# Kernel tuning notes

Measured on AMD Instinct MI355X. Metric: run time of the kernel, lower is better.

Reference implementation:

```python
import jax, jax.numpy as jnp
import numpy as np

# Dims
B, S, D = 2, 2048, 1024
H, KV = 16, 4            # rosa heads / kv heads -> n_rep = 4
QKB, VB = 16, 32          # query-key bits / value bits
N_REP = H // KV
TAU = 1.0


def setup_inputs() -> dict:
    key = jax.random.key(0)
    ks = jax.random.split(key, 8)
    sc = lambda fan_in: 1.0 / np.sqrt(fan_in)
    return {
        "hidden_states": jax.random.normal(ks[0], (B, S, D), jnp.float32),
        # Linear weights stored (in, out) so y = x @ W
        "Wq": jax.random.normal(ks[1], (D, H * QKB), jnp.float32) * sc(D),
        "Wk": jax.random.normal(ks[2], (D, KV * QKB), jnp.float32) * sc(D),
        "Wv": jax.random.normal(ks[3], (D, KV * VB), jnp.float32) * sc(D),
        "Wo": jax.random.normal(ks[4], (H * VB, D), jnp.float32) * sc(H * VB),
        "v_emb0": jnp.full((H * VB,), -1e-05, jnp.float32),
        "v_emb1": jnp.full((H * VB,), +1e-05, jnp.float32),
    }


def _repeat_kv(x, n_rep):
    # x: [B, KV, S, d] -> [B, KV*n_rep, S, d]
    b, kv, s, d = x.shape
    return jnp.broadcast_to(x[:, :, None], (b, kv, n_rep, s, d)).reshape(b, kv * n_rep, s, d)


def reference(hidden_states, Wq, Wk, Wv, Wo, v_emb0, v_emb1):
    b, s, _ = hidden_states.shape
    q = (hidden_states @ Wq).reshape(b, s, H, QKB).transpose(0, 2, 1, 3)   # [B,H,S,QKB]
    k = (hidden_states @ Wk).reshape(b, s, KV, QKB).transpose(0, 2, 1, 3)
    v = (hidden_states @ Wv).reshape(b, s, KV, VB).transpose(0, 2, 1, 3)
    k = _repeat_kv(k, N_REP)                                               # [B,H,S,QKB]
    v = _repeat_kv(v, N_REP)                                               # [B,H,S,VB]

    # Soft binarization (hard path uses (x > 0); soft path relaxes with sigmoid(x/tau)).
    pq = jax.nn.sigmoid(q / TAU)
    pk = jax.nn.sigmoid(k / TAU)
    pv = jax.nn.sigmoid(v / TAU)

    # Expected number of matching bits between soft-binary q_i and k_j:
    # sum_b [ pq*pk + (1-pq)(1-pk) ] = QKB - sum(pq) - sum(pk) + 2 * pq.pk
    dot = jnp.einsum("bhsd,bhtd->bhst", pq, pk)                            # [B,H,S,S]
    scores = QKB - pq.sum(-1)[:, :, :, None] - pk.sum(-1)[:, :, None, :] + 2.0 * dot

    causal = jnp.tril(jnp.ones((s, s), bool))                              # [S,S]
    scores = jnp.where(causal[None, None], scores, jnp.finfo(scores.dtype).min)
    attn = jax.nn.softmax(scores / TAU, axis=-1)

    vh = jnp.einsum("bhst,bhtd->bhsd", attn, pv)                           # [B,H,S,VB]
    e0 = v_emb0.reshape(1, H, 1, VB)
    e1 = v_emb1.reshape(1, H, 1, VB)
    out = e0 * (1.0 - vh) + e1 * vh                                        # [B,H,S,VB]
    out = out.transpose(0, 2, 1, 3).reshape(b, s, H * VB)
    return out @ Wo                                                        # [B,S,D]
```

## Files before the change

### kernel.cpp

```cpp
#include <hip/hip_runtime.h>
#include <hip/hip_bf16.h>

#define B_    2
#define S_    2048
#define D_    1024
#define H_    16
#define KV_   4
#define QKB_  16
#define VB_   32
#define NTOK  (B_ * S_)
#define L2E_  1.44269504088896f

typedef __attribute__((ext_vector_type(8))) short bshort8;
typedef __attribute__((ext_vector_type(4))) float f32x4;

__device__ __forceinline__ unsigned short bf16_rne(float x) {
    unsigned u = __float_as_uint(x);
    return (unsigned short)((u + 0x7FFFu + ((u >> 16) & 1u)) >> 16);
}
__device__ __forceinline__ unsigned bf16x2_rne(float lo, float hi) {
    return (unsigned)bf16_rne(lo) | ((unsigned)bf16_rne(hi) << 16);
}
__device__ __forceinline__ float sum2bf(unsigned u) {
    return __uint_as_float(u << 16) + __uint_as_float(u & 0xFFFF0000u);
}
__device__ __forceinline__ void stage16(const unsigned short* g, unsigned short* l) {
    __builtin_amdgcn_global_load_lds(
        (const __attribute__((address_space(1))) void*)g,
        (__attribute__((address_space(3))) void*)l, 16, 0, 0);
}

__global__ __launch_bounds__(256) void cvt_hs_kernel(
    const float* __restrict__ src, unsigned short* __restrict__ dst)
{
    int i = blockIdx.x * 256 + threadIdx.x;
    const float4* s = (const float4*)src;
    float4 a = s[2 * i], b = s[2 * i + 1];
    uint4 o;
    o.x = bf16x2_rne(a.x, a.y); o.y = bf16x2_rne(a.z, a.w);
    o.z = bf16x2_rne(b.x, b.y); o.w = bf16x2_rne(b.z, b.w);
    ((uint4*)dst)[i] = o;
}

__global__ __launch_bounds__(256) void trans_w_kernel(
    const float* __restrict__ Wq, const float* __restrict__ Wk,
    const float* __restrict__ Wv, const float* __restrict__ Wo,
    unsigned short* __restrict__ Wcat_t, unsigned short* __restrict__ Wot)
{
    __shared__ float T[64][65];
    const int bid = blockIdx.x, t = threadIdx.x;
    const float* src; unsigned short* dst; int K, N, tk, tn, drow0;
    if (bid < 64)       { src = Wq; dst = Wcat_t; K = 1024; N = 256;  int r = bid;       tk = r & 15; tn = r >> 4; drow0 = 0; }
    else if (bid < 80)  { src = Wk; dst = Wcat_t; K = 1024; N = 64;   int r = bid - 64;  tk = r;      tn = 0;      drow0 = 256; }
    else if (bid < 112) { src = Wv; dst = Wcat_t; K = 1024; N = 128;  int r = bid - 80;  tk = r & 15; tn = r >> 4; drow0 = 320; }
    else                { src = Wo; dst = Wot;    K = 512;  N = 1024; int r = bid - 112; tk = r & 7;  tn = r >> 3; drow0 = 0; }
    const int k0 = tk * 64, n0 = tn * 64;
    const int rr = t >> 4, cc = (t & 15) * 4;
    #pragma unroll
    for (int i = 0; i < 4; ++i) {
        float4 v = *(const float4*)(src + (k0 + rr + i * 16) * N + n0 + cc);
        T[rr + i * 16][cc + 0] = v.x; T[rr + i * 16][cc + 1] = v.y;
        T[rr + i * 16][cc + 2] = v.z; T[rr + i * 16][cc + 3] = v.w;
    }
    __syncthreads();
    const int nloc = t >> 2, kc = (t & 3) * 16;
    unsigned o[8];
    #pragma unroll
    for (int j = 0; j < 8; ++j)
        o[j] = bf16x2_rne(T[kc + 2 * j][nloc], T[kc + 2 * j + 1][nloc]);
    unsigned short* dp = dst + (drow0 + n0 + nloc) * K + k0 + kc;
    uint4 w0; w0.x = o[0]; w0.y = o[1]; w0.z = o[2]; w0.w = o[3];
    uint4 w1; w1.x = o[4]; w1.y = o[5]; w1.z = o[6]; w1.w = o[7];
    *(uint4*)(dp) = w0;
    *(uint4*)(dp + 8) = w1;
}

__global__ __launch_bounds__(256, 2) void proj_gemm(
    const unsigned short* __restrict__ Ab, const unsigned short* __restrict__ Btb,
    unsigned short* __restrict__ qg, unsigned short* __restrict__ pko,
    unsigned short* __restrict__ pvT)
{
    __shared__ unsigned short As[64 * 64];
    __shared__ unsigned short Bs[128 * 64];
    const int tid = threadIdx.x, l = tid & 63, w = tid >> 6;
    const int l15 = l & 15, quad = l >> 4;
    const int m0 = blockIdx.x * 64, n0 = blockIdx.y * 128;
    const int wr = w & 1, wc = w >> 1;
    const int sr8 = l >> 3, sc8 = l & 7;
    f32x4 c[2][4];
    #pragma unroll
    for (int i = 0; i < 2; ++i)
        #pragma unroll
        for (int j = 0; j < 4; ++j) c[i][j] = (f32x4){0.f, 0.f, 0.f, 0.f};

    for (int k0 = 0; k0 < 1024; k0 += 64) {
        {
            int R0 = w * 8, r0 = R0 + sr8;
            stage16(Ab + (m0 + r0) * 1024 + k0 + (sc8 ^ (r0 & 7)) * 8, &As[R0 * 64]);
            int R1 = 32 + w * 8, r1 = R1 + sr8;
            stage16(Ab + (m0 + r1) * 1024 + k0 + (sc8 ^ (r1 & 7)) * 8, &As[R1 * 64]);
        }
        #pragma unroll
        for (int j = 0; j < 4; ++j) {
            int R = j * 32 + w * 8, r = R + sr8;
            stage16(Btb + (n0 + r) * 1024 + k0 + (sc8 ^ (r & 7)) * 8, &Bs[R * 64]);
        }
        __syncthreads();
        #pragma unroll
        for (int kh = 0; kh < 2; ++kh) {
            bshort8 a[2], b[4];
            #pragma unroll
            for (int ar = 0; ar < 2; ++ar) {
                int row = wr * 32 + ar * 16 + l15;
                a[ar] = *(const bshort8*)&As[row * 64 + (((kh * 4 + quad) ^ (row & 7)) * 8)];
            }
            #pragma unroll
            for (int bc = 0; bc < 4; ++bc) {
                int row = wc * 64 + bc * 16 + l15;
                b[bc] = *(const bshort8*)&Bs[row * 64 + (((kh * 4 + quad) ^ (row & 7)) * 8)];
            }
            #pragma unroll
            for (int ar = 0; ar < 2; ++ar)
                #pragma unroll
                for (int bc = 0; bc < 4; ++bc)
                    c[ar][bc] = __builtin_amdgcn_mfma_f32_16x16x32_bf16(a[ar], b[bc], c[ar][bc], 0, 0, 0);
        }
        __syncthreads();
    }

    #pragma unroll
    for (int ar = 0; ar < 2; ++ar)
        #pragma unroll
        for (int bc = 0; bc < 4; ++bc) {
            f32x4 v = c[ar][bc];
            const int n = n0 + wc * 64 + bc * 16 + l15;
            if (n >= 448) continue;
            const int tok0 = m0 + wr * 32 + ar * 16 + quad * 4;
            float sg[4];
            #pragma unroll
            for (int r = 0; r < 4; ++r)
                sg[r] = 1.f / (1.f + exp2f(-v[r] * L2E_));
            if (n < 256) {
                const int hh = n >> 4, d = n & 15;
                #pragma unroll
                for (int r = 0; r < 4; ++r) {
                    int tok = tok0 + r, bb = tok >> 11, ss = tok & 2047;
                    qg[(((bb * 16 + hh) * 2048) + ss) * 16 + d] =
                        bf16_rne(L2E_ * (2.f * sg[r] - 1.f));
                }
            } else if (n < 320) {
                const int j = n - 256, kvv = j >> 4, d = j & 15;
                #pragma unroll
                for (int r = 0; r < 4; ++r) {
                    int tok = tok0 + r, bb = tok >> 11, ss = tok & 2047;
                    pko[(((bb * 4 + kvv) * 2048) + ss) * 16 + d] = bf16_rne(sg[r]);
                }
            } else {
                const int j = n - 320, kvv = j >> 5, d = j & 31;
                const int bb = tok0 >> 11, ss = tok0 & 2047;
                const int tl = ss >> 6, ccol = ss & 63;
                uint2 wv; wv.x = bf16x2_rne(sg[0], sg[1]); wv.y = bf16x2_rne(sg[2], sg[3]);
                *(uint2*)(pvT + ((((bb * 4 + kvv) * 32) + tl) * 32 + d) * 64 + ccol) = wv;
            }
        }
}

__global__ __launch_bounds__(256, 2) void outproj_gemm(
    const unsigned short* __restrict__ Ab, const unsigned short* __restrict__ Btb,
    float* __restrict__ out)
{
    __shared__ unsigned short As[128 * 64];
    __shared__ unsigned short Bs[128 * 64];
    const int tid = threadIdx.x, l = tid & 63, w = tid >> 6;
    const int l15 = l & 15, quad = l >> 4;
    const int m0 = blockIdx.x * 128, n0 = blockIdx.y * 128;
    const int wr = w & 1, wc = w >> 1;
    const int sr8 = l >> 3, sc8 = l & 7;
    f32x4 c[4][4];
    #pragma unroll
    for (int i = 0; i < 4; ++i)
        #pragma unroll
        for (int j = 0; j < 4; ++j) c[i][j] = (f32x4){0.f, 0.f, 0.f, 0.f};

    for (int k0 = 0; k0 < 512; k0 += 64) {
        #pragma unroll
        for (int j = 0; j < 4; ++j) {
            int R = j * 32 + w * 8, r = R + sr8;
            stage16(Ab  + (m0 + r) * 512 + k0 + (sc8 ^ (r & 7)) * 8, &As[R * 64]);
            stage16(Btb + (n0 + r) * 512 + k0 + (sc8 ^ (r & 7)) * 8, &Bs[R * 64]);
        }
        __syncthreads();
        #pragma unroll
        for (int kh = 0; kh < 2; ++kh) {
            bshort8 a[4], b[4];
            #pragma unroll
            for (int ar = 0; ar < 4; ++ar) {
                int row = wr * 64 + ar * 16 + l15;
                a[ar] = *(const bshort8*)&As[row * 64 + (((kh * 4 + quad) ^ (row & 7)) * 8)];
            }
            #pragma unroll
            for (int bc = 0; bc < 4; ++bc) {
                int row = wc * 64 + bc * 16 + l15;
                b[bc] = *(const bshort8*)&Bs[row * 64 + (((kh * 4 + quad) ^ (row & 7)) * 8)];
            }
            #pragma unroll
            for (int ar = 0; ar < 4; ++ar)
                #pragma unroll
                for (int bc = 0; bc < 4; ++bc)
                    c[ar][bc] = __builtin_amdgcn_mfma_f32_16x16x32_bf16(a[ar], b[bc], c[ar][bc], 0, 0, 0);
        }
        __syncthreads();
    }

    #pragma unroll
    for (int ar = 0; ar < 4; ++ar)
        #pragma unroll
        for (int bc = 0; bc < 4; ++bc) {
            f32x4 v = c[ar][bc];
            const int col = n0 + wc * 64 + bc * 16 + l15;
            const int r0 = m0 + wr * 64 + ar * 16 + quad * 4;
            #pragma unroll
            for (int r = 0; r < 4; ++r)
                out[(r0 + r) * D_ + col] = v[r];
        }
}

struct AttnLDS {
    unsigned short Kt[2][64][24];
    unsigned short qg[64][24];
    unsigned short P[4][16][88];
};

__global__ __launch_bounds__(256, 4) void attn_kernel(
    const unsigned short* __restrict__ qg_g, const unsigned short* __restrict__ pk_g,
    const unsigned short* __restrict__ pvT_g, const float* __restrict__ e0,
    const float* __restrict__ e1, unsigned short* __restrict__ xo)
{
    __shared__ AttnLDS L;
    const int tid = threadIdx.x, l = tid & 63, wq = tid >> 6;
    const int l15 = l & 15, quad = l >> 4;
    const int g = blockIdx.x;
    const int idx = g & 255, kg = g >> 8;
    const int bh = idx & 31, rr = idx >> 5;
    int qt;
    if      (kg == 0) qt = rr;
    else if (kg == 1) qt = 31 - rr;
    else if (kg == 2) qt = 8 + rr;
    else              qt = 23 - rr;
    const int b = bh >> 4, h = bh & 15, kv = h >> 2;
    const int qbase = qt * 64;
    const unsigned short* pkb = pk_g + ((b * 4 + kv) * 2048) * 16;
    const unsigned short* pvb = pvT_g + (b * 4 + kv) * 65536;
    const unsigned short* qgb = qg_g + ((b * 16 + h) * 2048) * 16;

    const f32x4 zero4 = {0.f, 0.f, 0.f, 0.f};
    const bshort8 zero8 = {0, 0, 0, 0, 0, 0, 0, 0};

    if (tid < 128) {
        int row = tid >> 1, half = tid & 1;
        *(uint4*)&L.qg[row][half * 8] = *(const uint4*)(qgb + (qbase + row) * 16 + half * 8);
        uint4 cst; cst.x = 0x3F80u; cst.y = 0u; cst.z = 0u; cst.w = 0u;
        *(uint4*)&L.Kt[tid >> 6][tid & 63][16] = cst;
    } else {
        int t2 = tid - 128, row = t2 >> 1, half = t2 & 1;
        *(uint4*)&L.Kt[0][row][half * 8] = *(const uint4*)(pkb + row * 16 + half * 8);
    }
    if (tid < 64) {
        const uint4* qp = (const uint4*)(qgb + (qbase + tid) * 16);
        uint4 u0 = qp[0], u1 = qp[1];
        float s = sum2bf(u0.x) + sum2bf(u0.y) + sum2bf(u0.z) + sum2bf(u0.w)
                + sum2bf(u1.x) + sum2bf(u1.y) + sum2bf(u1.z) + sum2bf(u1.w);
        uint4 sv; sv.x = (unsigned)bf16_rne(-8.f * L2E_ - 0.5f * s);
        sv.y = 0u; sv.z = 0u; sv.w = 0u;
        *(uint4*)&L.qg[tid][16] = sv;
    }
    __syncthreads();

    bshort8 qfrag = zero8;
    if (quad < 3) qfrag = *(const bshort8*)&L.qg[wq * 16 + l15][quad * 8];

    f32x4 acc0 = zero4, acc1 = zero4;
    float lsum = 0.f;

    for (int t = 0; t < qt; ++t) {
        if (tid < 128) {
            int row = tid >> 1, half = tid & 1;
            *(uint4*)&L.Kt[(t + 1) & 1][row][half * 8] =
                *(const uint4*)(pkb + ((t + 1) * 64 + row) * 16 + half * 8);
        }
        const unsigned short* Kb = &L.Kt[t & 1][0][0];
        const unsigned short* vb = pvb + t * 2048 + l15 * 64 + quad * 8;
        bshort8 vlo0 = *(const bshort8*)(vb);
        bshort8 vlo1 = *(const bshort8*)(vb + 32);
        bshort8 vhi0 = *(const bshort8*)(vb + 1024);
        bshort8 vhi1 = *(const bshort8*)(vb + 1056);

        f32x4 sc[4];
        #pragma unroll
        for (int ks = 0; ks < 4; ++ks) {
            bshort8 kf = zero8;
            if (quad < 3) kf = *(const bshort8*)(Kb + (ks * 16 + l15) * 24 + quad * 8);
            sc[ks] = __builtin_amdgcn_mfma_f32_16x16x32_bf16(kf, qfrag, zero4, 0, 0, 0);
        }
        #pragma unroll
        for (int ks = 0; ks < 4; ++ks) {
            float p0 = exp2f(sc[ks][0]), p1 = exp2f(sc[ks][1]);
            float p2 = exp2f(sc[ks][2]), p3 = exp2f(sc[ks][3]);
            lsum += p0 + p1 + p2 + p3;
            uint2 wv; wv.x = bf16x2_rne(p0, p1); wv.y = bf16x2_rne(p2, p3);
            *(uint2*)&L.P[wq][l15][ks * 16 + quad * 4] = wv;
        }
        {
            bshort8 pf0 = *(const bshort8*)&L.P[wq][l15][quad * 8];
            bshort8 pf1 = *(const bshort8*)&L.P[wq][l15][32 + quad * 8];
            acc0 = __builtin_amdgcn_mfma_f32_16x16x32_bf16(vlo0, pf0, acc0, 0, 0, 0);
            acc1 = __builtin_amdgcn_mfma_f32_16x16x32_bf16(vhi0, pf0, acc1, 0, 0, 0);
            acc0 = __builtin_amdgcn_mfma_f32_16x16x32_bf16(vlo1, pf1, acc0, 0, 0, 0);
            acc1 = __builtin_amdgcn_mfma_f32_16x16x32_bf16(vhi1, pf1, acc1, 0, 0, 0);
        }
        __syncthreads();
    }

    {
        const unsigned short* Kb = &L.Kt[qt & 1][0][0];
        const unsigned short* vb = pvb + qt * 2048 + l15 * 64 + quad * 8;
        bshort8 vlo0 = *(const bshort8*)(vb);
        bshort8 vlo1 = *(const bshort8*)(vb + 32);
        bshort8 vhi0 = *(const bshort8*)(vb + 1024);
        bshort8 vhi1 = *(const bshort8*)(vb + 1056);
        const int q_lane = qbase + wq * 16 + l15;

        f32x4 sc[4];
        #pragma unroll
        for (int ks = 0; ks < 4; ++ks) {
            bshort8 kf = zero8;
            if (quad < 3) kf = *(const bshort8*)(Kb + (ks * 16 + l15) * 24 + quad * 8);
            sc[ks] = __builtin_amdgcn_mfma_f32_16x16x32_bf16(kf, qfrag, zero4, 0, 0, 0);
        }
        #pragma unroll
        for (int ks = 0; ks < 4; ++ks) {
            float pv0[4];
            #pragma unroll
            for (int r = 0; r < 4; ++r) {
                const int tg = qbase + ks * 16 + quad * 4 + r;
                float pp = (tg <= q_lane) ? exp2f(sc[ks][r]) : 0.f;
                lsum += pp; pv0[r] = pp;
            }
            uint2 wv; wv.x = bf16x2_rne(pv0[0], pv0[1]); wv.y = bf16x2_rne(pv0[2], pv0[3]);
            *(uint2*)&L.P[wq][l15][ks * 16 + quad * 4] = wv;
        }
        {
            bshort8 pf0 = *(const bshort8*)&L.P[wq][l15][quad * 8];
            bshort8 pf1 = *(const bshort8*)&L.P[wq][l15][32 + quad * 8];
            acc0 = __builtin_amdgcn_mfma_f32_16x16x32_bf16(vlo0, pf0, acc0, 0, 0, 0);
            acc1 = __builtin_amdgcn_mfma_f32_16x16x32_bf16(vhi0, pf0, acc1, 0, 0, 0);
            acc0 = __builtin_amdgcn_mfma_f32_16x16x32_bf16(vlo1, pf1, acc0, 0, 0, 0);
            acc1 = __builtin_amdgcn_mfma_f32_16x16x32_bf16(vhi1, pf1, acc1, 0, 0, 0);
        }
    }

    lsum += __shfl_xor(lsum, 16);
    lsum += __shfl_xor(lsum, 32);
    const float inv = 1.f / lsum;

    float e0v[8], dEv[8];
    #pragma unroll
    for (int vs = 0; vs < 2; ++vs)
        #pragma unroll
        for (int r = 0; r < 4; ++r) {
            int idx2 = h * 32 + vs * 16 + quad * 4 + r;
            float a = e0[idx2];
            e0v[vs * 4 + r] = a; dEv[vs * 4 + r] = e1[idx2] - a;
        }
    const int tok = b * 2048 + qbase + wq * 16 + l15;
    float o0[4], o1[4];
    #pragma unroll
    for (int r = 0; r < 4; ++r) {
        o0[r] = e0v[r]     + dEv[r]     * (acc0[r] * inv);
        o1[r] = e0v[4 + r] + dEv[4 + r] * (acc1[r] * inv);
    }
    uint2 w0; w0.x = bf16x2_rne(o0[0], o0[1]); w0.y = bf16x2_rne(o0[2], o0[3]);
    uint2 w1; w1.x = bf16x2_rne(o1[0], o1[1]); w1.y = bf16x2_rne(o1[2], o1[3]);
    *(uint2*)(xo + tok * 512 + h * 32 + quad * 4)      = w0;
    *(uint2*)(xo + tok * 512 + h * 32 + 16 + quad * 4) = w1;
}

extern "C" void kernel_launch(void* const* d_in, const int* in_sizes, int n_in,
                              void* d_out, int out_size, void* d_ws, size_t ws_size,
                              hipStream_t stream)
{
    const float* hs = (const float*)d_in[0];
    const float* Wq = (const float*)d_in[1];
    const float* Wk = (const float*)d_in[2];
    const float* Wv = (const float*)d_in[3];
    const float* Wo = (const float*)d_in[4];
    const float* e0 = (const float*)d_in[5];
    const float* e1 = (const float*)d_in[6];
    float* out = (float*)d_out;

    char* ws = (char*)d_ws;
    unsigned short* hs_b   = (unsigned short*)(ws);
    unsigned short* xo     = (unsigned short*)(ws);
    unsigned short* Wcat_t = (unsigned short*)(ws + 8388608);
    unsigned short* Wot    = (unsigned short*)(ws + 8388608 + 917504);
    unsigned short* qg     = (unsigned short*)(ws + 10354688);
    unsigned short* pk     = (unsigned short*)(ws + 12451840);
    unsigned short* pvT    = (unsigned short*)(ws + 12976128);

    cvt_hs_kernel<<<2048, 256, 0, stream>>>(hs, hs_b);
    trans_w_kernel<<<240, 256, 0, stream>>>(Wq, Wk, Wv, Wo, Wcat_t, Wot);
    proj_gemm<<<dim3(64, 4), 256, 0, stream>>>(hs_b, Wcat_t, qg, pk, pvT);
    attn_kernel<<<1024, 256, 0, stream>>>(qg, pk, pvT, e0, e1, xo);
    outproj_gemm<<<dim3(32, 8), 256, 0, stream>>>(xo, Wot, out);
}
```

Measured before the change: 147.0 us.

## Merge prep kernels, retile projection GEMMs, and drop LDS staging in attention

Fuses the hidden-state conversion and weight-transpose kernels into a single prep launch to save one kernel launch. Retiles the QKV projection to 64x64 tiles on a 64x7 grid so no padded columns are computed, and halves the out-projection M tile to 64 on a 64x8 grid to launch more blocks. In the attention kernel, Q and K fragments are now read straight from global memory into registers instead of being staged through LDS, which removes the per-tile __syncthreads. The trade-offs are lower per-block data reuse in the GEMMs and reliance on cache for the K loads.

```diff
diff --git a/kernel.cpp b/kernel.cpp
--- a/kernel.cpp
+++ b/kernel.cpp
@@ -30,25 +30,26 @@
         (__attribute__((address_space(3))) void*)l, 16, 0, 0);
 }
 
-__global__ __launch_bounds__(256) void cvt_hs_kernel(
-    const float* __restrict__ src, unsigned short* __restrict__ dst)
-{
-    int i = blockIdx.x * 256 + threadIdx.x;
-    const float4* s = (const float4*)src;
-    float4 a = s[2 * i], b = s[2 * i + 1];
-    uint4 o;
-    o.x = bf16x2_rne(a.x, a.y); o.y = bf16x2_rne(a.z, a.w);
-    o.z = bf16x2_rne(b.x, b.y); o.w = bf16x2_rne(b.z, b.w);
-    ((uint4*)dst)[i] = o;
-}
-
-__global__ __launch_bounds__(256) void trans_w_kernel(
+__global__ __launch_bounds__(256) void prep_kernel(
+    const float* __restrict__ hs,
     const float* __restrict__ Wq, const float* __restrict__ Wk,
     const float* __restrict__ Wv, const float* __restrict__ Wo,
+    unsigned short* __restrict__ hs_b,
     unsigned short* __restrict__ Wcat_t, unsigned short* __restrict__ Wot)
 {
     __shared__ float T[64][65];
-    const int bid = blockIdx.x, t = threadIdx.x;
+    const int t = threadIdx.x;
+    if (blockIdx.x < 2048) {
+        int i = blockIdx.x * 256 + t;
+        const float4* s = (const float4*)hs;
+        float4 a = s[2 * i], b = s[2 * i + 1];
+        uint4 o;
+        o.x = bf16x2_rne(a.x, a.y); o.y = bf16x2_rne(a.z, a.w);
+        o.z = bf16x2_rne(b.x, b.y); o.w = bf16x2_rne(b.z, b.w);
+        ((uint4*)hs_b)[i] = o;
+        return;
+    }
+    const int bid = blockIdx.x - 2048;
     const float* src; unsigned short* dst; int K, N, tk, tn, drow0;
     if (bid < 64)       { src = Wq; dst = Wcat_t; K = 1024; N = 256;  int r = bid;       tk = r & 15; tn = r >> 4; drow0 = 0; }
     else if (bid < 80)  { src = Wk; dst = Wcat_t; K = 1024; N = 64;   int r = bid - 64;  tk = r;      tn = 0;      drow0 = 256; }
@@ -75,10 +76,80 @@
     *(uint4*)(dp + 8) = w1;
 }
 
-__global__ __launch_bounds__(256, 2) void proj_gemm(
+__global__ __launch_bounds__(256, 4) void proj_gemm(
     const unsigned short* __restrict__ Ab, const unsigned short* __restrict__ Btb,
     unsigned short* __restrict__ qg, unsigned short* __restrict__ pko,
     unsigned short* __restrict__ pvT)
+{
+    __shared__ unsigned short As[64 * 64];
+    __shared__ unsigned short Bs[64 * 64];
+    const int tid = threadIdx.x, l = tid & 63, w = tid >> 6;
+    const int l15 = l & 15, quad = l >> 4;
+    const int m0 = blockIdx.x * 64, n0 = blockIdx.y * 64;
+    const int sr8 = l >> 3, sc8 = l & 7;
+    f32x4 c[4];
+    #pragma unroll
+    for (int j = 0; j < 4; ++j) c[j] = (f32x4){0.f, 0.f, 0.f, 0.f};
+
+    for (int k0 = 0; k0 < 1024; k0 += 64) {
+        int R0 = w * 8, r0 = R0 + sr8;
+        int R1 = 32 + w * 8, r1 = R1 + sr8;
+        stage16(Ab  + (m0 + r0) * 1024 + k0 + (sc8 ^ (r0 & 7)) * 8, &As[R0 * 64]);
+        stage16(Ab  + (m0 + r1) * 1024 + k0 + (sc8 ^ (r1 & 7)) * 8, &As[R1 * 64]);
+        stage16(Btb + (n0 + r0) * 1024 + k0 + (sc8 ^ (r0 & 7)) * 8, &Bs[R0 * 64]);
+        stage16(Btb + (n0 + r1) * 1024 + k0 + (sc8 ^ (r1 & 7)) * 8, &Bs[R1 * 64]);
+        __syncthreads();
+        #pragma unroll
+        for (int kh = 0; kh < 2; ++kh) {
+            const int arow = w * 16 + l15;
+            bshort8 a = *(const bshort8*)&As[arow * 64 + (((kh * 4 + quad) ^ (arow & 7)) * 8)];
+            #pragma unroll
+            for (int bc = 0; bc < 4; ++bc) {
+                const int brow = bc * 16 + l15;
+                bshort8 b = *(const bshort8*)&Bs[brow * 64 + (((kh * 4 + quad) ^ (brow & 7)) * 8)];
+                c[bc] = __builtin_amdgcn_mfma_f32_16x16x32_bf16(a, b, c[bc], 0, 0, 0);
+            }
+        }
+        __syncthreads();
+    }
+
+    const int tok0 = m0 + w * 16 + quad * 4;
+    #pragma unroll
+    for (int bc = 0; bc < 4; ++bc) {
+        f32x4 v = c[bc];
+        const int n = n0 + bc * 16 + l15;
+        float sg[4];
+        #pragma unroll
+        for (int r = 0; r < 4; ++r)
+            sg[r] = 1.f / (1.f + exp2f(-v[r] * L2E_));
+        if (n < 256) {
+            const int hh = n >> 4, d = n & 15;
+            #pragma unroll
+            for (int r = 0; r < 4; ++r) {
+                int tok = tok0 + r, bb = tok >> 11, ss = tok & 2047;
+                qg[(((bb * 16 + hh) * 2048) + ss) * 16 + d] =
+                    bf16_rne(L2E_ * (2.f * sg[r] - 1.f));
+            }
+        } else if (n < 320) {
+            const int j = n - 256, kvv = j >> 4, d = j & 15;
+            #pragma unroll
+            for (int r = 0; r < 4; ++r) {
+                int tok = tok0 + r, bb = tok >> 11, ss = tok & 2047;
+                pko[(((bb * 4 + kvv) * 2048) + ss) * 16 + d] = bf16_rne(sg[r]);
+            }
+        } else {
+            const int j = n - 320, kvv = j >> 5, d = j & 31;
+            const int bb = tok0 >> 11, ss = tok0 & 2047;
+            const int tl = ss >> 6, ccol = ss & 63;
+            uint2 wv; wv.x = bf16x2_rne(sg[0], sg[1]); wv.y = bf16x2_rne(sg[2], sg[3]);
+            *(uint2*)(pvT + ((((bb * 4 + kvv) * 32) + tl) * 32 + d) * 64 + ccol) = wv;
+        }
+    }
+}
+
+__global__ __launch_bounds__(256, 2) void outproj_gemm(
+    const unsigned short* __restrict__ Ab, const unsigned short* __restrict__ Btb,
+    float* __restrict__ out)
 {
     __shared__ unsigned short As[64 * 64];
     __shared__ unsigned short Bs[128 * 64];
@@ -93,17 +164,16 @@
         #pragma unroll
         for (int j = 0; j < 4; ++j) c[i][j] = (f32x4){0.f, 0.f, 0.f, 0.f};
 
-    for (int k0 = 0; k0 < 1024; k0 += 64) {
-        {
-            int R0 = w * 8, r0 = R0 + sr8;
-            stage16(Ab + (m0 + r0) * 1024 + k0 + (sc8 ^ (r0 & 7)) * 8, &As[R0 * 64]);
-            int R1 = 32 + w * 8, r1 = R1 + sr8;
-            stage16(Ab + (m0 + r1) * 1024 + k0 + (sc8 ^ (r1 & 7)) * 8, &As[R1 * 64]);
+    for (int k0 = 0; k0 < 512; k0 += 64) {
+        #pragma unroll
+        for (int j = 0; j < 2; ++j) {
+            int R = w * 16 + j * 8, r = R + sr8;
+            stage16(Ab + (m0 + r) * 512 + k0 + (sc8 ^ (r & 7)) * 8, &As[R * 64]);
         }
         #pragma unroll
         for (int j = 0; j < 4; ++j) {
             int R = j * 32 + w * 8, r = R + sr8;
-            stage16(Btb + (n0 + r) * 1024 + k0 + (sc8 ^ (r & 7)) * 8, &Bs[R * 64]);
+            stage16(Btb + (n0 + r) * 512 + k0 + (sc8 ^ (r & 7)) * 8, &Bs[R * 64]);
         }
         __syncthreads();
         #pragma unroll
@@ -133,92 +203,8 @@
         #pragma unroll
         for (int bc = 0; bc < 4; ++bc) {
             f32x4 v = c[ar][bc];
-            const int n = n0 + wc * 64 + bc * 16 + l15;
-            if (n >= 448) continue;
-            const int tok0 = m0 + wr * 32 + ar * 16 + quad * 4;
-            float sg[4];
-            #pragma unroll
-            for (int r = 0; r < 4; ++r)
-                sg[r] = 1.f / (1.f + exp2f(-v[r] * L2E_));
-            if (n < 256) {
-                const int hh = n >> 4, d = n & 15;
-                #pragma unroll
-                for (int r = 0; r < 4; ++r) {
-                    int tok = tok0 + r, bb = tok >> 11, ss = tok & 2047;
-                    qg[(((bb * 16 + hh) * 2048) + ss) * 16 + d] =
-                        bf16_rne(L2E_ * (2.f * sg[r] - 1.f));
-                }
-            } else if (n < 320) {
-                const int j = n - 256, kvv = j >> 4, d = j & 15;
-                #pragma unroll
-                for (int r = 0; r < 4; ++r) {
-                    int tok = tok0 + r, bb = tok >> 11, ss = tok & 2047;
-                    pko[(((bb * 4 + kvv) * 2048) + ss) * 16 + d] = bf16_rne(sg[r]);
-                }
-            } else {
-                const int j = n - 320, kvv = j >> 5, d = j & 31;
-                const int bb = tok0 >> 11, ss = tok0 & 2047;
-                const int tl = ss >> 6, ccol = ss & 63;
-                uint2 wv; wv.x = bf16x2_rne(sg[0], sg[1]); wv.y = bf16x2_rne(sg[2], sg[3]);
-                *(uint2*)(pvT + ((((bb * 4 + kvv) * 32) + tl) * 32 + d) * 64 + ccol) = wv;
-            }
-        }
-}
-
-__global__ __launch_bounds__(256, 2) void outproj_gemm(
-    const unsigned short* __restrict__ Ab, const unsigned short* __restrict__ Btb,
-    float* __restrict__ out)
-{
-    __shared__ unsigned short As[128 * 64];
-    __shared__ unsigned short Bs[128 * 64];
-    const int tid = threadIdx.x, l = tid & 63, w = tid >> 6;
-    const int l15 = l & 15, quad = l >> 4;
-    const int m0 = blockIdx.x * 128, n0 = blockIdx.y * 128;
-    const int wr = w & 1, wc = w >> 1;
-    const int sr8 = l >> 3, sc8 = l & 7;
-    f32x4 c[4][4];
-    #pragma unroll
-    for (int i = 0; i < 4; ++i)
-        #pragma unroll
-        for (int j = 0; j < 4; ++j) c[i][j] = (f32x4){0.f, 0.f, 0.f, 0.f};
-
-    for (int k0 = 0; k0 < 512; k0 += 64) {
-        #pragma unroll
-        for (int j = 0; j < 4; ++j) {
-            int R = j * 32 + w * 8, r = R + sr8;
-            stage16(Ab  + (m0 + r) * 512 + k0 + (sc8 ^ (r & 7)) * 8, &As[R * 64]);
-            stage16(Btb + (n0 + r) * 512 + k0 + (sc8 ^ (r & 7)) * 8, &Bs[R * 64]);
-        }
-        __syncthreads();
-        #pragma unroll
-        for (int kh = 0; kh < 2; ++kh) {
-            bshort8 a[4], b[4];
-            #pragma unroll
-            for (int ar = 0; ar < 4; ++ar) {
-                int row = wr * 64 + ar * 16 + l15;
-                a[ar] = *(const bshort8*)&As[row * 64 + (((kh * 4 + quad) ^ (row & 7)) * 8)];
-            }
-            #pragma unroll
-            for (int bc = 0; bc < 4; ++bc) {
-                int row = wc * 64 + bc * 16 + l15;
-                b[bc] = *(const bshort8*)&Bs[row * 64 + (((kh * 4 + quad) ^ (row & 7)) * 8)];
-            }
-            #pragma unroll
-            for (int ar = 0; ar < 4; ++ar)
-                #pragma unroll
-                for (int bc = 0; bc < 4; ++bc)
-                    c[ar][bc] = __builtin_amdgcn_mfma_f32_16x16x32_bf16(a[ar], b[bc], c[ar][bc], 0, 0, 0);
-        }
-        __syncthreads();
-    }
-
-    #pragma unroll
-    for (int ar = 0; ar < 4; ++ar)
-        #pragma unroll
-        for (int bc = 0; bc < 4; ++bc) {
-            f32x4 v = c[ar][bc];
             const int col = n0 + wc * 64 + bc * 16 + l15;
-            const int r0 = m0 + wr * 64 + ar * 16 + quad * 4;
+            const int r0 = m0 + wr * 32 + ar * 16 + quad * 4;
             #pragma unroll
             for (int r = 0; r < 4; ++r)
                 out[(r0 + r) * D_ + col] = v[r];
@@ -226,8 +212,6 @@
 }
 
 struct AttnLDS {
-    unsigned short Kt[2][64][24];
-    unsigned short qg[64][24];
     unsigned short P[4][16][88];
 };
 
@@ -256,52 +240,38 @@
     const f32x4 zero4 = {0.f, 0.f, 0.f, 0.f};
     const bshort8 zero8 = {0, 0, 0, 0, 0, 0, 0, 0};
 
-    if (tid < 128) {
-        int row = tid >> 1, half = tid & 1;
-        *(uint4*)&L.qg[row][half * 8] = *(const uint4*)(qgb + (qbase + row) * 16 + half * 8);
-        uint4 cst; cst.x = 0x3F80u; cst.y = 0u; cst.z = 0u; cst.w = 0u;
-        *(uint4*)&L.Kt[tid >> 6][tid & 63][16] = cst;
-    } else {
-        int t2 = tid - 128, row = t2 >> 1, half = t2 & 1;
-        *(uint4*)&L.Kt[0][row][half * 8] = *(const uint4*)(pkb + row * 16 + half * 8);
-    }
-    if (tid < 64) {
-        const uint4* qp = (const uint4*)(qgb + (qbase + tid) * 16);
-        uint4 u0 = qp[0], u1 = qp[1];
-        float s = sum2bf(u0.x) + sum2bf(u0.y) + sum2bf(u0.z) + sum2bf(u0.w)
-                + sum2bf(u1.x) + sum2bf(u1.y) + sum2bf(u1.z) + sum2bf(u1.w);
-        uint4 sv; sv.x = (unsigned)bf16_rne(-8.f * L2E_ - 0.5f * s);
-        sv.y = 0u; sv.z = 0u; sv.w = 0u;
-        *(uint4*)&L.qg[tid][16] = sv;
-    }
-    __syncthreads();
-
+    const unsigned short* qrow = qgb + (qbase + wq * 16 + l15) * 16;
+    uint4 qu0 = *(const uint4*)qrow;
+    uint4 qu1 = *(const uint4*)(qrow + 8);
+    float s = sum2bf(qu0.x) + sum2bf(qu0.y) + sum2bf(qu0.z) + sum2bf(qu0.w)
+            + sum2bf(qu1.x) + sum2bf(qu1.y) + sum2bf(qu1.z) + sum2bf(qu1.w);
     bshort8 qfrag = zero8;
-    if (quad < 3) qfrag = *(const bshort8*)&L.qg[wq * 16 + l15][quad * 8];
+    if (quad == 0)      qfrag = __builtin_bit_cast(bshort8, qu0);
+    else if (quad == 1) qfrag = __builtin_bit_cast(bshort8, qu1);
+    else if (quad == 2) qfrag[0] = (short)bf16_rne(-8.f * L2E_ - 0.5f * s);
+
+    bshort8 kone = zero8; kone[0] = (short)0x3F80;
 
     f32x4 acc0 = zero4, acc1 = zero4;
     float lsum = 0.f;
 
     for (int t = 0; t < qt; ++t) {
-        if (tid < 128) {
-            int row = tid >> 1, half = tid & 1;
-            *(uint4*)&L.Kt[(t + 1) & 1][row][half * 8] =
-                *(const uint4*)(pkb + ((t + 1) * 64 + row) * 16 + half * 8);
-        }
-        const unsigned short* Kb = &L.Kt[t & 1][0][0];
+        const int t0 = t * 64;
+        f32x4 sc[4];
+        #pragma unroll
+        for (int ks = 0; ks < 4; ++ks) {
+            bshort8 kf;
+            if (quad < 2)       kf = *(const bshort8*)(pkb + (t0 + ks * 16 + l15) * 16 + quad * 8);
+            else if (quad == 2) kf = kone;
+            else                kf = zero8;
+            sc[ks] = __builtin_amdgcn_mfma_f32_16x16x32_bf16(kf, qfrag, zero4, 0, 0, 0);
+        }
         const unsigned short* vb = pvb + t * 2048 + l15 * 64 + quad * 8;
         bshort8 vlo0 = *(const bshort8*)(vb);
         bshort8 vlo1 = *(const bshort8*)(vb + 32);
         bshort8 vhi0 = *(const bshort8*)(vb + 1024);
         bshort8 vhi1 = *(const bshort8*)(vb + 1056);
 
-        f32x4 sc[4];
-        #pragma unroll
-        for (int ks = 0; ks < 4; ++ks) {
-            bshort8 kf = zero8;
-            if (quad < 3) kf = *(const bshort8*)(Kb + (ks * 16 + l15) * 24 + quad * 8);
-            sc[ks] = __builtin_amdgcn_mfma_f32_16x16x32_bf16(kf, qfrag, zero4, 0, 0, 0);
-        }
         #pragma unroll
         for (int ks = 0; ks < 4; ++ks) {
             float p0 = exp2f(sc[ks][0]), p1 = exp2f(sc[ks][1]);
@@ -318,31 +288,32 @@
             acc0 = __builtin_amdgcn_mfma_f32_16x16x32_bf16(vlo1, pf1, acc0, 0, 0, 0);
             acc1 = __builtin_amdgcn_mfma_f32_16x16x32_bf16(vhi1, pf1, acc1, 0, 0, 0);
         }
-        __syncthreads();
     }
 
     {
-        const unsigned short* Kb = &L.Kt[qt & 1][0][0];
+        const int t0 = qt * 64;
+        const int q_lane = qbase + wq * 16 + l15;
+        f32x4 sc[4];
+        #pragma unroll
+        for (int ks = 0; ks < 4; ++ks) {
+            bshort8 kf;
+            if (quad < 2)       kf = *(const bshort8*)(pkb + (t0 + ks * 16 + l15) * 16 + quad * 8);
+            else if (quad == 2) kf = kone;
+            else                kf = zero8;
+            sc[ks] = __builtin_amdgcn_mfma_f32_16x16x32_bf16(kf, qfrag, zero4, 0, 0, 0);
+        }
         const unsigned short* vb = pvb + qt * 2048 + l15 * 64 + quad * 8;
         bshort8 vlo0 = *(const bshort8*)(vb);
         bshort8 vlo1 = *(const bshort8*)(vb + 32);
         bshort8 vhi0 = *(const bshort8*)(vb + 1024);
         bshort8 vhi1 = *(const bshort8*)(vb + 1056);
-        const int q_lane = qbase + wq * 16 + l15;
-
-        f32x4 sc[4];
-        #pragma unroll
-        for (int ks = 0; ks < 4; ++ks) {
-            bshort8 kf = zero8;
-            if (quad < 3) kf = *(const bshort8*)(Kb + (ks * 16 + l15) * 24 + quad * 8);
-            sc[ks] = __builtin_amdgcn_mfma_f32_16x16x32_bf16(kf, qfrag, zero4, 0, 0, 0);
-        }
+
         #pragma unroll
         for (int ks = 0; ks < 4; ++ks) {
             float pv0[4];
             #pragma unroll
             for (int r = 0; r < 4; ++r) {
-                const int tg = qbase + ks * 16 + quad * 4 + r;
+                const int tg = t0 + ks * 16 + quad * 4 + r;
                 float pp = (tg <= q_lane) ? exp2f(sc[ks][r]) : 0.f;
                 lsum += pp; pv0[r] = pp;
             }
@@ -407,9 +378,8 @@
     unsigned short* pk     = (unsigned short*)(ws + 12451840);
     unsigned short* pvT    = (unsigned short*)(ws + 12976128);
 
-    cvt_hs_kernel<<<2048, 256, 0, stream>>>(hs, hs_b);
-    trans_w_kernel<<<240, 256, 0, stream>>>(Wq, Wk, Wv, Wo, Wcat_t, Wot);
-    proj_gemm<<<dim3(64, 4), 256, 0, stream>>>(hs_b, Wcat_t, qg, pk, pvT);
+    prep_kernel<<<2288, 256, 0, stream>>>(hs, Wq, Wk, Wv, Wo, hs_b, Wcat_t, Wot);
+    proj_gemm<<<dim3(64, 7), 256, 0, stream>>>(hs_b, Wcat_t, qg, pk, pvT);
     attn_kernel<<<1024, 256, 0, stream>>>(qg, pk, pvT, e0, e1, xo);
-    outproj_gemm<<<dim3(32, 8), 256, 0, stream>>>(xo, Wot, out);
-}
+    outproj_gemm<<<dim3(64, 8), 256, 0, stream>>>(xo, Wot, out);
+}
```

After: 158.7 us. +7.9%, slower.
